# Kernel tuning notes

Measured on AMD Instinct MI355X. Metric: run time of the kernel, lower is better.

The kernel has to match this reference:

```python
import jax, jax.numpy as jnp
import numpy as np

B, T, C, H = 8, 2048, 1024, 16
N_LAYER, LAYER_ID = 12, 1
NH = C // H           # head size = 64
CHUNK = 256


def setup_inputs() -> dict:
    key = jax.random.key(0)
    ks = jax.random.split(key, 10)
    # deterministic init matching the torch __init__
    ratio_0_to_1 = LAYER_ID / (N_LAYER - 1)
    ratio_1_to_almost0 = 1.0 - LAYER_ID / N_LAYER
    ddd = np.arange(C, dtype=np.float32) / C
    time_maa_k = (1.0 - ddd ** ratio_1_to_almost0).astype(np.float32)
    time_maa_v = (1.0 - (ddd ** ratio_1_to_almost0 + 0.3 * ratio_0_to_1)).astype(np.float32)
    time_maa_r = (1.0 - ddd ** (0.5 * ratio_1_to_almost0)).astype(np.float32)
    h_idx = np.arange(H, dtype=np.float32)
    time_decay = (-6.0 + 5.0 * (h_idx / (H - 1)) ** (0.7 + 1.3 * ratio_0_to_1)).astype(np.float32)
    s = 0.02
    return {
        "x": jax.random.normal(ks[0], (B, T, C), jnp.float32),
        "volatility": jax.random.uniform(ks[1], (B, T), jnp.float32),
        "Wvol": jax.random.normal(ks[2], (C, 1), jnp.float32) * s,
        "bvol": jnp.zeros((C,), jnp.float32),
        "time_maa_k": jnp.asarray(time_maa_k),
        "time_maa_v": jnp.asarray(time_maa_v),
        "time_maa_r": jnp.asarray(time_maa_r),
        "time_decay": jnp.asarray(time_decay),
        "Wk": jax.random.normal(ks[3], (C, C), jnp.float32) * s,
        "Wv": jax.random.normal(ks[4], (C, C), jnp.float32) * s,
        "Wr": jax.random.normal(ks[5], (C, C), jnp.float32) * s,
        "Wo": jax.random.normal(ks[6], (C, C), jnp.float32) * s,
        "gn_w": 1.0 + jax.random.normal(ks[7], (C,), jnp.float32) * s,
        "gn_b": jax.random.normal(ks[8], (C,), jnp.float32) * s,
    }


def reference(x, volatility, Wvol, bvol, time_maa_k, time_maa_v, time_maa_r,
              time_decay, Wk, Wv, Wr, Wo, gn_w, gn_b):
    b, t, c = x.shape
    h = time_decay.shape[0]
    n = c // h
    nc = t // CHUNK

    # volatility gating: sigmoid(Linear(1->C))
    v_emb = jax.nn.sigmoid(volatility[:, :, None] * Wvol[:, 0] + bvol)  # (B,T,C)
    x = x * v_emb

    # time shift (zero-pad one step at the front, drop last)
    xx = jnp.pad(x, ((0, 0), (1, 0), (0, 0)))[:, :-1] - x
    xk = x + xx * time_maa_k
    xv = x + xx * time_maa_v
    xr = x + xx * time_maa_r

    r = (xr @ Wr.T).reshape(b, t, h, n).transpose(0, 2, 1, 3)  # (B,H,T,N)
    k = (xk @ Wk.T).reshape(b, t, h, n).transpose(0, 2, 1, 3)
    v = (xv @ Wv.T).reshape(b, t, h, n).transpose(0, 2, 1, 3)

    w = jnp.exp(-jnp.exp(time_decay))[None, :, None, None]  # scalar decay per head

    # chunked linear-attention recurrence (faithful to torch loop, chunk=256, no intra-chunk mask)
    rc = r.reshape(b, h, nc, CHUNK, n).transpose(2, 0, 1, 3, 4)  # (nc,B,H,CK,N)
    kc = k.reshape(b, h, nc, CHUNK, n).transpose(2, 0, 1, 3, 4)
    vc = v.reshape(b, h, nc, CHUNK, n).transpose(2, 0, 1, 3, 4)

    def step(state, rkv):
        rr, kk, vv = rkv  # each (B,H,CK,N)
        att = jnp.einsum('bhtn,bhsn->bhts', rr, kk)            # r @ k^T
        y = w * (jnp.einsum('bhts,bhsn->bhtn', att, vv)
                 + jnp.einsum('bhtn,bhnm->bhtm', rr, state))
        new_state = w * (state + jnp.einsum('bhsn,bhsm->bhnm', kk, vv))
        return new_state, y

    state0 = jnp.zeros((b, h, n, n), x.dtype)
    _, ys = jax.lax.scan(step, state0, (rc, kc, vc))            # (nc,B,H,CK,N)
    y = ys.transpose(1, 2, 0, 3, 4).reshape(b, h, t, n)
    y = y.transpose(0, 2, 1, 3).reshape(b * t, c)

    # GroupNorm with H groups over channels
    yg = y.reshape(b * t, h, n)
    mu = yg.mean(-1, keepdims=True)
    var = yg.var(-1, keepdims=True)
    yg = (yg - mu) * jax.lax.rsqrt(var + 1e-5)
    y = (yg.reshape(b * t, c) * gn_w + gn_b).reshape(b, t, c)

    return y @ Wo.T  # dropout is identity in eval
```

## Files before the change

### kernel.cpp

```cpp
#include <hip/hip_runtime.h>

typedef unsigned short u16;
typedef __attribute__((ext_vector_type(4))) unsigned int u32x4;
typedef __attribute__((ext_vector_type(4))) float f32x4;
typedef __attribute__((ext_vector_type(8))) short s16x8;

#define B_ 8
#define T_ 2048
#define C_ 1024
#define H_ 16
#define HS_ 64
#define CHUNK_ 256
#define NC_ 8

union U8 { u32x4 u; u16 h[8]; };

__device__ __forceinline__ float b2f(u16 v) {
    union { unsigned int i; float f; } c; c.i = ((unsigned int)v) << 16; return c.f;
}
__device__ __forceinline__ u16 f2b(float f) {
    union { float f; unsigned int i; } c; c.f = f;
    unsigned int i = c.i;
    return (u16)((i + 0x7FFFu + ((i >> 16) & 1u)) >> 16);
}
__device__ __forceinline__ float fsig(float z) {
    return __builtin_amdgcn_rcpf(1.f + __expf(-z));
}

typedef __attribute__((address_space(1))) void GV;
typedef __attribute__((address_space(3))) void LV;
__device__ __forceinline__ void glds16(const void* g, void* l) {
    __builtin_amdgcn_global_load_lds((GV*)g, (LV*)l, 16, 0, 0);
}

__global__ __launch_bounds__(256) void cvt4_kernel(
    const float* __restrict__ s0, const float* __restrict__ s1,
    const float* __restrict__ s2, const float* __restrict__ s3,
    u16* __restrict__ dst)
{
    int i = blockIdx.x * 256 + threadIdx.x;
    int m = i >> 17;
    const float* s = (m == 0) ? s0 : (m == 1) ? s1 : (m == 2) ? s2 : s3;
    size_t j = (size_t)(i & 131071) * 8;
    f32x4 a = *reinterpret_cast<const f32x4*>(s + j);
    f32x4 b = *reinterpret_cast<const f32x4*>(s + j + 4);
    U8 o;
    #pragma unroll
    for (int k = 0; k < 4; k++) { o.h[k] = f2b(a[k]); o.h[4 + k] = f2b(b[k]); }
    *reinterpret_cast<u32x4*>(dst + (size_t)m * C_ * C_ + j) = o.u;
}

__global__ __launch_bounds__(256) void mix_kernel(
    const float* __restrict__ x, const float* __restrict__ vol,
    const float* __restrict__ Wvol, const float* __restrict__ bvol,
    const float* __restrict__ mk, const float* __restrict__ mv, const float* __restrict__ mr,
    u16* __restrict__ xk, u16* __restrict__ xv, u16* __restrict__ xr)
{
    int idx = blockIdx.x * 256 + threadIdx.x;
    int c0 = (idx & 127) * 8;
    int bt4 = idx >> 7;
    int t0  = (bt4 & 511) * 4;
    int b   = bt4 >> 9;
    size_t rowOff = ((size_t)b * T_ + t0) * C_ + c0;

    float wv[8], bv[8], mkv[8], mvv[8], mrv[8];
    #pragma unroll
    for (int j = 0; j < 8; j += 4) {
        f32x4 a;
        a = *reinterpret_cast<const f32x4*>(Wvol + c0 + j);
        wv[j] = a[0]; wv[j+1] = a[1]; wv[j+2] = a[2]; wv[j+3] = a[3];
        a = *reinterpret_cast<const f32x4*>(bvol + c0 + j);
        bv[j] = a[0]; bv[j+1] = a[1]; bv[j+2] = a[2]; bv[j+3] = a[3];
        a = *reinterpret_cast<const f32x4*>(mk + c0 + j);
        mkv[j] = a[0]; mkv[j+1] = a[1]; mkv[j+2] = a[2]; mkv[j+3] = a[3];
        a = *reinterpret_cast<const f32x4*>(mv + c0 + j);
        mvv[j] = a[0]; mvv[j+1] = a[1]; mvv[j+2] = a[2]; mvv[j+3] = a[3];
        a = *reinterpret_cast<const f32x4*>(mr + c0 + j);
        mrv[j] = a[0]; mrv[j+1] = a[1]; mrv[j+2] = a[2]; mrv[j+3] = a[3];
    }

    const float* volb = vol + (size_t)b * T_;
    float gp[8];
    if (t0 == 0) {
        #pragma unroll
        for (int j = 0; j < 8; j++) gp[j] = 0.f;
    } else {
        float vp = volb[t0 - 1];
        #pragma unroll
        for (int j = 0; j < 8; j += 4) {
            f32x4 a = *reinterpret_cast<const f32x4*>(x + rowOff - C_ + j);
            gp[j]   = a[0] * fsig(vp * wv[j]   + bv[j]);
            gp[j+1] = a[1] * fsig(vp * wv[j+1] + bv[j+1]);
            gp[j+2] = a[2] * fsig(vp * wv[j+2] + bv[j+2]);
            gp[j+3] = a[3] * fsig(vp * wv[j+3] + bv[j+3]);
        }
    }

    #pragma unroll
    for (int s = 0; s < 4; s++) {
        float vc = volb[t0 + s];
        size_t off = rowOff + (size_t)s * C_;
        float g[8];
        #pragma unroll
        for (int j = 0; j < 8; j += 4) {
            f32x4 a = *reinterpret_cast<const f32x4*>(x + off + j);
            g[j]   = a[0] * fsig(vc * wv[j]   + bv[j]);
            g[j+1] = a[1] * fsig(vc * wv[j+1] + bv[j+1]);
            g[j+2] = a[2] * fsig(vc * wv[j+2] + bv[j+2]);
            g[j+3] = a[3] * fsig(vc * wv[j+3] + bv[j+3]);
        }
        U8 ok, ov, orr;
        #pragma unroll
        for (int j = 0; j < 8; j++) {
            float xx = gp[j] - g[j];
            ok.h[j]  = f2b(g[j] + xx * mkv[j]);
            ov.h[j]  = f2b(g[j] + xx * mvv[j]);
            orr.h[j] = f2b(g[j] + xx * mrv[j]);
            gp[j] = g[j];
        }
        *reinterpret_cast<u32x4*>(xk + off) = ok.u;
        *reinterpret_cast<u32x4*>(xv + off) = ov.u;
        *reinterpret_cast<u32x4*>(xr + off) = orr.u;
    }
}

#define GBM_ 256
#define GBN_ 256
#define GBK_ 64
#define GK_  1024
#define GNT_ 16
#define GEMM_LDS_BYTES 131072

template<int MODE>
__global__ __launch_bounds__(512, 2) void gemm_bt(
    const u16* __restrict__ A, const u16* __restrict__ W, void* __restrict__ Cc)
{
    extern __shared__ __align__(16) u16 lds[];
    const int tid  = threadIdx.x;
    const int lane = tid & 63, w = tid >> 6;
    const int r16  = lane & 15, quad = lane >> 4;
    const int wm2  = w >> 2;
    const int wn4  = w & 3;
    const int id   = blockIdx.x;
    const int bm   = id & 63, bn = id >> 6;

    const u16* Ab = A + (size_t)bm * GBM_ * GK_;
    const u16* Wb = W + (size_t)bn * GBN_ * GK_;

    const int srow8  = lane >> 3;
    const int schunk = ((lane & 7) ^ srow8) * 8;
    const u16* aSrc = Ab + (size_t)(w * 16 + srow8) * GK_ + schunk;
    const u16* bSrc = Wb + (size_t)(w * 16 + srow8) * GK_ + schunk;

    const int fA0 = (wm2 * 128 + r16) * 64;
    const int fB0 = 16384 + (wn4 * 64 + r16) * 64;
    const int c0 = ((quad)     ^ (r16 & 7)) * 8;
    const int c1 = ((quad | 4) ^ (r16 & 7)) * 8;

    f32x4 acc[8][4];
    #pragma unroll
    for (int mi = 0; mi < 8; mi++)
        #pragma unroll
        for (int ni = 0; ni < 4; ni++)
            acc[mi][ni] = f32x4{0.f, 0.f, 0.f, 0.f};

#define STQ(tt, h) do {                                                       \
    const size_t ko_ = (size_t)(tt) * 64;                                     \
    u16* db_ = lds + (((tt) & 1) * 32768) + ((h) * 128 + w * 16) * 64;        \
    glds16(aSrc + (size_t)((h) * 128)     * GK_ + ko_, db_);                  \
    glds16(aSrc + (size_t)((h) * 128 + 8) * GK_ + ko_, db_ + 512);            \
    glds16(bSrc + (size_t)((h) * 128)     * GK_ + ko_, db_ + 16384);          \
    glds16(bSrc + (size_t)((h) * 128 + 8) * GK_ + ko_, db_ + 16384 + 512);    \
} while (0)

#define PH_BAR() do { asm volatile("" ::: "memory");                          \
    __builtin_amdgcn_s_barrier(); asm volatile("" ::: "memory"); } while (0)
#define PH_LGKM0() do { asm volatile("s_waitcnt lgkmcnt(0)" ::: "memory");    \
    __builtin_amdgcn_sched_barrier(0); } while (0)
#define LDFA(CO) { _Pragma("unroll") for (int mi = 0; mi < 8; mi++)           \
    fa[mi] = *reinterpret_cast<const s16x8*>(lds + pb + fA0 + mi * 1024 + (CO)); }
#define LDFB(NH, CO) { _Pragma("unroll") for (int ni = 0; ni < 2; ni++)       \
    fb[ni] = *reinterpret_cast<const s16x8*>(lds + pb + fB0 + ((NH) * 2 + ni) * 1024 + (CO)); }
#define MFMA16(NH) do { __builtin_amdgcn_s_setprio(1);                        \
    _Pragma("unroll") for (int mi = 0; mi < 8; mi++) {                        \
        acc[mi][(NH)*2+0] = __builtin_amdgcn_mfma_f32_16x16x32_bf16(          \
            fa[mi], fb[0], acc[mi][(NH)*2+0], 0, 0, 0);                       \
        acc[mi][(NH)*2+1] = __builtin_amdgcn_mfma_f32_16x16x32_bf16(          \
            fa[mi], fb[1], acc[mi][(NH)*2+1], 0, 0, 0);                       \
    } __builtin_amdgcn_s_setprio(0); } while (0)

    STQ(0, 0);
    STQ(0, 1);
    asm volatile("s_waitcnt vmcnt(0)" ::: "memory");
    PH_BAR();

    for (int t = 0; t < GNT_; ++t) {
        const int pb = (t & 1) * 32768;
        s16x8 fa[8], fb[2];
        LDFA(c0); LDFB(0, c0);
        if (t + 1 < GNT_) { STQ(t + 1, 0); STQ(t + 1, 1); }
        PH_BAR(); PH_LGKM0(); MFMA16(0); PH_BAR();
        LDFB(1, c0);
        PH_BAR(); PH_LGKM0(); MFMA16(1); PH_BAR();
        LDFA(c1); LDFB(0, c1);
        PH_BAR(); PH_LGKM0(); MFMA16(0); PH_BAR();
        LDFB(1, c1);
        PH_BAR(); PH_LGKM0(); MFMA16(1);
        asm volatile("s_waitcnt vmcnt(0)" ::: "memory");
        PH_BAR();
    }
#undef STQ
#undef LDFA
#undef LDFB
#undef MFMA16
#undef PH_LGKM0
#undef PH_BAR

    if constexpr (MODE == 0) {
        float* C = (float*)Cc;
        #pragma unroll
        for (int mi = 0; mi < 8; mi++) {
            int row0 = bm * GBM_ + wm2 * 128 + mi * 16 + quad * 4;
            #pragma unroll
            for (int ni = 0; ni < 4; ni++) {
                int col = bn * GBN_ + wn4 * 64 + ni * 16 + r16;
                #pragma unroll
                for (int i = 0; i < 4; i++)
                    C[(size_t)(row0 + i) * C_ + col] = acc[mi][ni][i];
            }
        }
    } else if constexpr (MODE == 1) {
        u16* ep = lds + w * 4608;
        u16* C = (u16*)Cc;
        #pragma unroll
        for (int half = 0; half < 2; half++) {
            #pragma unroll
            for (int mi2 = 0; mi2 < 4; mi2++) {
                int mi = half * 4 + mi2;
                #pragma unroll
                for (int ni = 0; ni < 4; ni++)
                    #pragma unroll
                    for (int i = 0; i < 4; i++)
                        ep[(mi2 * 16 + quad * 4 + i) * 72 + ni * 16 + r16] =
                            f2b(acc[mi][ni][i]);
            }
            asm volatile("s_waitcnt lgkmcnt(0)" ::: "memory");
            __builtin_amdgcn_sched_barrier(0);
            #pragma unroll
            for (int it = 0; it < 8; it++) {
                int rr = it * 8 + (lane >> 3);
                u32x4 val = *reinterpret_cast<const u32x4*>(ep + rr * 72 + (lane & 7) * 8);
                size_t grow = (size_t)(bm * GBM_ + wm2 * 128 + half * 64 + rr);
                *reinterpret_cast<u32x4*>(
                    C + grow * C_ + bn * GBN_ + wn4 * 64 + (lane & 7) * 8) = val;
            }
            asm volatile("s_waitcnt vmcnt(0) lgkmcnt(0)" ::: "memory");
        }
    } else {
        u16* ep = lds + w * 8192;
        #pragma unroll
        for (int mi = 0; mi < 8; mi++) {
            const int chunk = mi * 2 + (quad >> 1);
            const int rsub = (quad & 1) * 4;
            #pragma unroll
            for (int ni = 0; ni < 4; ni++) {
                const int col = ni * 16 + r16;
                u16* p = ep + col * 128 + ((chunk ^ col) & 15) * 8 + rsub;
                p[0] = f2b(acc[mi][ni][0]);
                p[1] = f2b(acc[mi][ni][1]);
                p[2] = f2b(acc[mi][ni][2]);
                p[3] = f2b(acc[mi][ni][3]);
            }
        }
        asm volatile("s_waitcnt lgkmcnt(0)" ::: "memory");
        __builtin_amdgcn_sched_barrier(0);
        u16* C = (u16*)Cc;
        const int cl = lane >> 2, ch4 = lane & 3;
        const int gc0 = bn * 16 + wn4 * 4;
        const int tt0 = bm * 8 + wm2 * 4;
        #pragma unroll
        for (int it = 0; it < 16; it++) {
            const int col_l = (it & 3) * 16 + cl;
            const int chunk = (it >> 2) * 4 + ch4;
            u32x4 val = *reinterpret_cast<const u32x4*>(
                ep + col_l * 128 + ((chunk ^ col_l) & 15) * 8);
            const size_t tile = (size_t)(gc0 + (it & 3)) * 512 + tt0 + (it >> 2);
            *reinterpret_cast<u32x4*>(C + tile * 512 + cl * 32 + ch4 * 8) = val;
        }
    }
}

#define KVS_LDS_BYTES 98304

__global__ __launch_bounds__(512) void kvscan_kernel(
    const u16* __restrict__ kT, const u16* __restrict__ vT,
    const float* __restrict__ td, u16* __restrict__ stT)
{
    extern __shared__ __align__(16) u16 klds[];
    const int bm2 = blockIdx.x;
    const int mh = bm2 & 1, bh = bm2 >> 1;
    const int h = bh & (H_ - 1), b = bh >> 4;
    const float wdec = expf(-expf(td[h]));
    const int tid = threadIdx.x, lane = tid & 63, w = tid >> 6;
    const int r16 = lane & 15, quad = lane >> 4;
    const int cgn = w >> 1;
    const int ck  = w & 1;
    const int tt0 = b * 64;
    const int loff = r16 * 32 + quad * 8;

#define KSTG(jj, bb) do {                                                     \
    u16* db_ = klds + (bb) * 24576;                                           \
    _Pragma("unroll")                                                         \
    for (int q = 0; q < 6; q++) {                                             \
        const int tau = w * 6 + q;                                            \
        const u16* src;                                                       \
        if (tau < 32)                                                         \
            src = vT + ((size_t)(h * 4 + (tau >> 3)) * 512 +                  \
                        tt0 + (jj) * 8 + (tau & 7)) * 512;                    \
        else                                                                  \
            src = kT + ((size_t)(h * 4 + mh * 2 + ((tau - 32) >> 3)) * 512 +  \
                        tt0 + (jj) * 8 + ((tau - 32) & 7)) * 512;             \
        glds16(src + (size_t)lane * 8, db_ + tau * 512);                      \
    }                                                                         \
} while (0)

    KSTG(0, 0);

    f32x4 st = f32x4{0.f, 0.f, 0.f, 0.f};
    for (int j = 0; j < NC_; ++j) {
        asm volatile("s_waitcnt vmcnt(0)" ::: "memory");
        __syncthreads();
        if (j + 1 < NC_) KSTG(j + 1, (j + 1) & 1);
        const u16* bb = klds + (j & 1) * 24576;
        f32x4 acc = f32x4{0.f, 0.f, 0.f, 0.f};
        #pragma unroll
        for (int ks = 0; ks < 8; ks++) {
            s16x8 fa = *reinterpret_cast<const s16x8*>(
                bb + (cgn * 8 + ks) * 512 + loff);
            s16x8 fb = *reinterpret_cast<const s16x8*>(
                bb + (32 + ck * 8 + ks) * 512 + loff);
            acc = __builtin_amdgcn_mfma_f32_16x16x32_bf16(fa, fb, acc, 0, 0, 0);
        }
        st = (st + acc) * wdec;
        u16* out = stT + ((size_t)bh * NC_ + j) * 4096;
        #pragma unroll
        for (int i = 0; i < 4; i++)
            out[(cgn * 16 + quad * 4 + i) * HS_ + mh * 32 + ck * 16 + r16] =
                f2b(st[i]);
    }
#undef KSTG
}

__global__ __launch_bounds__(256) void rstate_gn_kernel(
    const u16* __restrict__ r, const u16* __restrict__ stT,
    const float* __restrict__ gnw, const float* __restrict__ gnb, u16* __restrict__ ygn)
{
    int blk = blockIdx.x;
    int c  = blk & (NC_ - 1);
    int bh = blk >> 3;
    int h = bh & (H_ - 1);
    int b = bh >> 4;
    __shared__ __align__(16) u16 sT[HS_ * 72];
    int tid = threadIdx.x, lane = tid & 63, wave = tid >> 6;
    int r16 = lane & 15, quad = lane >> 4;

    const u16* sg = stT + (size_t)blk * (HS_ * HS_);
    for (int i = tid; i < 512; i += 256) {
        int n = i >> 3, c8 = (i & 7) * 8;
        *reinterpret_cast<u32x4*>(&sT[n * 72 + c8]) =
            *reinterpret_cast<const u32x4*>(sg + n * HS_ + c8);
    }
    __syncthreads();

    size_t rowBase = (size_t)(b * T_ + c * CHUNK_ + wave * 64);
    f32x4 acc[4][4];
    #pragma unroll
    for (int mi = 0; mi < 4; mi++)
        #pragma unroll
        for (int ni = 0; ni < 4; ni++)
            acc[mi][ni] = f32x4{0.f, 0.f, 0.f, 0.f};

    #pragma unroll
    for (int ks = 0; ks < 2; ks++) {
        int kb = ks * 32 + quad * 8;
        s16x8 fa[4], fb[4];
        #pragma unroll
        for (int mi = 0; mi < 4; mi++)
            fa[mi] = *reinterpret_cast<const s16x8*>(
                r + (rowBase + mi * 16 + r16) * C_ + h * HS_ + kb);
        #pragma unroll
        for (int ni = 0; ni < 4; ni++)
            fb[ni] = *reinterpret_cast<const s16x8*>(&sT[(ni * 16 + r16) * 72 + kb]);
        #pragma unroll
        for (int mi = 0; mi < 4; mi++)
            #pragma unroll
            for (int ni = 0; ni < 4; ni++)
                acc[mi][ni] = __builtin_amdgcn_mfma_f32_16x16x32_bf16(fa[mi], fb[ni], acc[mi][ni], 0, 0, 0);
    }

    float gwv[4], gbv[4];
    #pragma unroll
    for (int ni = 0; ni < 4; ni++) {
        int col = ni * 16 + r16;
        gwv[ni] = gnw[h * HS_ + col];
        gbv[ni] = gnb[h * HS_ + col];
    }
    #pragma unroll
    for (int mi = 0; mi < 4; mi++) {
        float s1[4], s2[4];
        #pragma unroll
        for (int i = 0; i < 4; i++) {
            float s = 0.f, ss = 0.f;
            #pragma unroll
            for (int ni = 0; ni < 4; ni++) {
                float v = acc[mi][ni][i];
                s += v; ss += v * v;
            }
            s1[i] = s; s2[i] = ss;
        }
        #pragma unroll
        for (int d = 1; d < 16; d <<= 1) {
            #pragma unroll
            for (int i = 0; i < 4; i++) {
                s1[i] += __shfl_xor(s1[i], d);
                s2[i] += __shfl_xor(s2[i], d);
            }
        }
        #pragma unroll
        for (int i = 0; i < 4; i++) {
            float mu = s1[i] * (1.f / 64.f);
            float var = s2[i] * (1.f / 64.f) - mu * mu;
            float sc = rsqrtf(var + 1e-5f);
            size_t ob = (rowBase + mi * 16 + quad * 4 + i) * C_ + h * HS_;
            #pragma unroll
            for (int ni = 0; ni < 4; ni++)
                ygn[ob + ni * 16 + r16] = f2b((acc[mi][ni][i] - mu) * sc * gwv[ni] + gbv[ni]);
        }
    }
}

extern "C" void kernel_launch(void* const* d_in, const int* in_sizes, int n_in,
                              void* d_out, int out_size, void* d_ws, size_t ws_size,
                              hipStream_t stream) {
    const float* x    = (const float*)d_in[0];
    const float* vol  = (const float*)d_in[1];
    const float* Wvol = (const float*)d_in[2];
    const float* bvol = (const float*)d_in[3];
    const float* mk   = (const float*)d_in[4];
    const float* mv   = (const float*)d_in[5];
    const float* mr   = (const float*)d_in[6];
    const float* td   = (const float*)d_in[7];
    const float* Wk   = (const float*)d_in[8];
    const float* Wv   = (const float*)d_in[9];
    const float* Wr   = (const float*)d_in[10];
    const float* Wo   = (const float*)d_in[11];
    const float* gnw  = (const float*)d_in[12];
    const float* gnb  = (const float*)d_in[13];
    float* out = (float*)d_out;

    static bool init_attr = []() {
        hipFuncSetAttribute(reinterpret_cast<const void*>(gemm_bt<0>),
                            hipFuncAttributeMaxDynamicSharedMemorySize, GEMM_LDS_BYTES);
        hipFuncSetAttribute(reinterpret_cast<const void*>(gemm_bt<1>),
                            hipFuncAttributeMaxDynamicSharedMemorySize, GEMM_LDS_BYTES);
        hipFuncSetAttribute(reinterpret_cast<const void*>(gemm_bt<2>),
                            hipFuncAttributeMaxDynamicSharedMemorySize, GEMM_LDS_BYTES);
        hipFuncSetAttribute(reinterpret_cast<const void*>(kvscan_kernel),
                            hipFuncAttributeMaxDynamicSharedMemorySize, KVS_LDS_BYTES);
        return true;
    }();
    (void)init_attr;

    char* ws = (char*)d_ws;
    const size_t SLOT = (size_t)B_ * T_ * C_ * 2;
    u16* xr = (u16*)(ws + 0 * SLOT);
    u16* xk = (u16*)(ws + 1 * SLOT);
    u16* xv = (u16*)(ws + 2 * SLOT);
    u16* rb = (u16*)(ws + 3 * SLOT);
    u16* kbT = (u16*)(ws + 0 * SLOT);
    u16* vbT = (u16*)(ws + 1 * SLOT);
    u16* stT = (u16*)(ws + 2 * SLOT + SLOT / 2);
    u16* ygn = (u16*)(ws + 0 * SLOT);
    u16* wtb = (u16*)(ws + 4 * SLOT);
    u16* wrb = wtb;
    u16* wkb = wrb + (size_t)C_ * C_;
    u16* wvb = wkb + (size_t)C_ * C_;
    u16* wob = wvb + (size_t)C_ * C_;

    cvt4_kernel<<<dim3(4 * (C_ * C_ / 8) / 256), dim3(256), 0, stream>>>(Wr, Wk, Wv, Wo, wtb);

    mix_kernel<<<dim3(2048), dim3(256), 0, stream>>>(
        x, vol, Wvol, bvol, mk, mv, mr, xk, xv, xr);

    gemm_bt<1><<<dim3(256), dim3(512), GEMM_LDS_BYTES, stream>>>(xr, wrb, rb);
    gemm_bt<2><<<dim3(256), dim3(512), GEMM_LDS_BYTES, stream>>>(xk, wkb, kbT);
    gemm_bt<2><<<dim3(256), dim3(512), GEMM_LDS_BYTES, stream>>>(xv, wvb, vbT);

    kvscan_kernel<<<dim3(B_ * H_ * 2), dim3(512), KVS_LDS_BYTES, stream>>>(kbT, vbT, td, stT);

    rstate_gn_kernel<<<dim3(B_ * H_ * NC_), dim3(256), 0, stream>>>(rb, stT, gnw, gnb, ygn);

    gemm_bt<0><<<dim3(256), dim3(512), GEMM_LDS_BYTES, stream>>>(ygn, wob, out);
}
```

Before: 346.0 us.

## Split GEMM tile loads into staggered A/B stages with partial vmcnt waits

Restructures the double-buffered GEMM main loop so the next tile's A and B global-to-LDS loads are issued in separate pieces between MFMA phases, with B rows assigned in interleaved groups. Partial vmcnt waits replace the full drain at the end of each iteration, and several barriers are removed. The goal is to overlap memory traffic with MFMA work and cut synchronisation stalls. The cost is more fragile ordering: correctness relies on the vmcnt counts matching the number of outstanding loads and on the barrier placement still protecting buffer reuse.

```diff
diff --git a/kernel.cpp b/kernel.cpp
--- a/kernel.cpp
+++ b/kernel.cpp
@@ -149,14 +149,18 @@
 
     const int srow8  = lane >> 3;
     const int schunk = ((lane & 7) ^ srow8) * 8;
-    const u16* aSrc = Ab + (size_t)(w * 16 + srow8) * GK_ + schunk;
-    const u16* bSrc = Wb + (size_t)(w * 16 + srow8) * GK_ + schunk;
+    const u16* aSrc  = Ab + (size_t)(w * 16 + srow8) * GK_ + schunk;
+    const u16* bSrcR = Wb + (size_t)srow8 * GK_ + schunk;
 
     const int fA0 = (wm2 * 128 + r16) * 64;
     const int fB0 = 16384 + (wn4 * 64 + r16) * 64;
     const int c0 = ((quad)     ^ (r16 & 7)) * 8;
     const int c1 = ((quad | 4) ^ (r16 & 7)) * 8;
 
+    const int i0_ = w * 2, i1_ = w * 2 + 1;
+    const int rB0 = (i0_ >> 2) * 64 + (i0_ & 3) * 8;
+    const int rB1 = (i1_ >> 2) * 64 + (i1_ & 3) * 8;
+
     f32x4 acc[8][4];
     #pragma unroll
     for (int mi = 0; mi < 8; mi++)
@@ -164,13 +168,21 @@
         for (int ni = 0; ni < 4; ni++)
             acc[mi][ni] = f32x4{0.f, 0.f, 0.f, 0.f};
 
-#define STQ(tt, h) do {                                                       \
+#define SQA(tt) do {                                                          \
     const size_t ko_ = (size_t)(tt) * 64;                                     \
-    u16* db_ = lds + (((tt) & 1) * 32768) + ((h) * 128 + w * 16) * 64;        \
-    glds16(aSrc + (size_t)((h) * 128)     * GK_ + ko_, db_);                  \
-    glds16(aSrc + (size_t)((h) * 128 + 8) * GK_ + ko_, db_ + 512);            \
-    glds16(bSrc + (size_t)((h) * 128)     * GK_ + ko_, db_ + 16384);          \
-    glds16(bSrc + (size_t)((h) * 128 + 8) * GK_ + ko_, db_ + 16384 + 512);    \
+    u16* db_ = lds + (((tt) & 1) * 32768) + w * 1024;                         \
+    glds16(aSrc + ko_,                 db_);                                  \
+    glds16(aSrc + 8   * GK_ + ko_,     db_ + 512);                            \
+    glds16(aSrc + 128 * GK_ + ko_,     db_ + 8192);                           \
+    glds16(aSrc + 136 * GK_ + ko_,     db_ + 8192 + 512);                     \
+} while (0)
+
+#define SQB(tt, hi) do {                                                      \
+    const size_t ko_ = (size_t)(tt) * 64;                                     \
+    u16* bb_ = lds + (((tt) & 1) * 32768) + 16384;                            \
+    const int ra_ = rB0 + (hi) * 32, rb_ = rB1 + (hi) * 32;                   \
+    glds16(bSrcR + (size_t)ra_ * GK_ + ko_, bb_ + ra_ * 64);                  \
+    glds16(bSrcR + (size_t)rb_ * GK_ + ko_, bb_ + rb_ * 64);                  \
 } while (0)
 
 #define PH_BAR() do { asm volatile("" ::: "memory");                          \
@@ -189,32 +201,41 @@
             fa[mi], fb[1], acc[mi][(NH)*2+1], 0, 0, 0);                       \
     } __builtin_amdgcn_s_setprio(0); } while (0)
 
-    STQ(0, 0);
-    STQ(0, 1);
-    asm volatile("s_waitcnt vmcnt(0)" ::: "memory");
-    PH_BAR();
+    SQA(0); SQB(0, 0); SQB(0, 1);
 
     for (int t = 0; t < GNT_; ++t) {
         const int pb = (t & 1) * 32768;
         s16x8 fa[8], fb[2];
+        asm volatile("s_waitcnt vmcnt(2)" ::: "memory");
+        PH_BAR();
         LDFA(c0); LDFB(0, c0);
-        if (t + 1 < GNT_) { STQ(t + 1, 0); STQ(t + 1, 1); }
-        PH_BAR(); PH_LGKM0(); MFMA16(0); PH_BAR();
+        if (t + 1 < GNT_) SQA(t + 1);
+        PH_LGKM0(); MFMA16(0);
+        if (t + 1 < GNT_) asm volatile("s_waitcnt vmcnt(4)" ::: "memory");
+        else              asm volatile("s_waitcnt vmcnt(0)" ::: "memory");
+        PH_BAR();
         LDFB(1, c0);
-        PH_BAR(); PH_LGKM0(); MFMA16(1); PH_BAR();
+        if (t + 1 < GNT_) SQB(t + 1, 0);
+        PH_LGKM0(); MFMA16(1);
         LDFA(c1); LDFB(0, c1);
-        PH_BAR(); PH_LGKM0(); MFMA16(0); PH_BAR();
+        PH_BAR();
+        if (t + 1 < GNT_) SQB(t + 1, 1);
+        PH_LGKM0(); MFMA16(0);
         LDFB(1, c1);
-        PH_BAR(); PH_LGKM0(); MFMA16(1);
-        asm volatile("s_waitcnt vmcnt(0)" ::: "memory");
         PH_BAR();
-    }
-#undef STQ
+        PH_LGKM0(); MFMA16(1);
+    }
+#undef SQA
+#undef SQB
 #undef LDFA
 #undef LDFB
 #undef MFMA16
 #undef PH_LGKM0
 #undef PH_BAR
+
+    asm volatile("s_waitcnt vmcnt(0)" ::: "memory");
+    __builtin_amdgcn_s_barrier();
+    asm volatile("" ::: "memory");
 
     if constexpr (MODE == 0) {
         float* C = (float*)Cc;
```

After: 329.5 us. -4.7%, faster.
